# Performance work log

Hardware: AMD Instinct MI355X
Metric: run time of the kernel (lower is better)

The kernel has to match this reference:

```python
import jax, jax.numpy as jnp
import numpy as np

PI = 3.141592653589793
EPSILON = 1e-3
USE_TANH = True


def setup_inputs() -> dict:
    key = jax.random.key(0)
    k1, k2, k3, k4, k5 = jax.random.split(key, 5)
    b, t, d, p = 4, 8192, 64, 8
    return {
        "query": jax.random.normal(k1, (b, t, d), dtype=jnp.float32),
        "W_Q": jax.random.normal(k2, (p, d), dtype=jnp.float32),
        "W_K": jax.random.normal(k3, (p, d), dtype=jnp.float32),
        "W_V": jax.random.normal(k4, (p, d, d), dtype=jnp.float32),
        "W_O": jax.random.uniform(k5, (p,), dtype=jnp.float32),
    }


def reference(query, W_Q, W_K, W_V, W_O):
    # key = value = query (decoder-only self-attention usage)
    q = jnp.einsum("bti,pi->btp", query, W_Q)
    k = jnp.einsum("bti,pi->btp", query, W_K)
    V = jnp.einsum("bti,pio->btpo", query, W_V)  # (b,t,p,o)
    if USE_TANH:
        q = jnp.tanh(q) * (PI / 4)
        k = jnp.tanh(k) * (PI / 4)
    cos_k = jnp.cos(k)[..., None]  # (b,t,p,1)
    sin_k = jnp.sin(k)[..., None]
    # causal prefix sums over time (axis=-3)
    cos_KV = jnp.cumsum(cos_k * V, axis=-3)
    sin_KV = jnp.cumsum(sin_k * V, axis=-3)
    cos_Q = jnp.cos(q)[..., None]
    sin_Q = jnp.sin(q)[..., None]
    heads = cos_Q * cos_KV + sin_Q * sin_KV  # (b,t,p,o)
    cos_K = jnp.cumsum(cos_k, axis=-3)
    sin_K = jnp.cumsum(sin_k, axis=-3)
    denom = cos_Q * cos_K + sin_Q * sin_K + EPSILON
    heads = heads / denom
    return jnp.einsum("btpo,p->bto", heads, W_O)
```

## Files before the change

### kernel.cpp

```cpp
#include <hip/hip_runtime.h>
#include <hip/hip_bf16.h>
#include <math.h>

#define BB  4
#define TT  8192
#define DD  64
#define PP  8
#define CC  32
#define NCH (TT/CC)
#define AGG_STRIDE 130
#define QSTR 68

#define EPSV 1e-3f
#define KPI4 0.78539816339744830962f

typedef __attribute__((ext_vector_type(8))) short short8;
typedef __attribute__((ext_vector_type(4))) float f32x4;

__device__ __forceinline__ float bf2f(unsigned short h) {
  return __uint_as_float(((unsigned)h) << 16);
}
__device__ __forceinline__ unsigned short f2bf(float f) {
  unsigned u = __float_as_uint(f);
  u += 0x7fffu + ((u >> 16) & 1u);
  return (unsigned short)(u >> 16);
}
__device__ __forceinline__ float fast_tanh(float x) {
  float e = __expf(2.f * x);
  return 1.f - 2.f * __builtin_amdgcn_rcpf(e + 1.f);
}

__global__ __launch_bounds__(256) void k_pass1(const float* __restrict__ q,
                                               const float* __restrict__ Wk,
                                               const float* __restrict__ Wv,
                                               float* __restrict__ agg,
                                               unsigned short* __restrict__ WvTh,
                                               unsigned short* __restrict__ WvTl) {
  const int blk = blockIdx.x;
  const int c = blk & (NCH - 1);
  const int b = blk >> 8;

  __shared__ float SH[64 * QSTR];
  __shared__ float Wks[PP * DD];
  __shared__ float2 kts[PP * 32];

  const int tid = threadIdx.x;
  const float* qb = q + ((size_t)b * TT + (size_t)c * CC) * DD;
  for (int g = tid; g < CC * DD; g += 256) SH[(g >> 6) * QSTR + (g & 63)] = qb[g];
  for (int g = tid; g < PP * DD; g += 256) Wks[g] = Wk[g];
  __syncthreads();

  {
    const int t = tid & 31, p = tid >> 5;
    float dk = 0.f;
    const float4* qr = (const float4*)&SH[t * QSTR];
    const float4* wr = (const float4*)&Wks[p * DD];
#pragma unroll
    for (int j = 0; j < 16; ++j) {
      float4 qv = qr[j], wv = wr[j];
      dk = fmaf(qv.x, wv.x, dk); dk = fmaf(qv.y, wv.y, dk);
      dk = fmaf(qv.z, wv.z, dk); dk = fmaf(qv.w, wv.w, dk);
    }
    float ang = fast_tanh(dk) * KPI4;
    float ck = __cosf(ang), sk = __sinf(ang);
    kts[p * 32 + t] = make_float2(ck, sk);
    float rc = ck, rs = sk;
#pragma unroll
    for (int d = 16; d >= 1; d >>= 1) {
      rc += __shfl_xor(rc, d, 32);
      rs += __shfl_xor(rs, d, 32);
    }
    if (t == 0)
      *(float2*)(agg + (size_t)((b * PP + p) * NCH + c) * AGG_STRIDE + 128) =
          make_float2(rc, rs);
  }
  __syncthreads();

  {
    const int i = tid & 63, pq = tid >> 6;
    const int p0 = pq, p1 = pq + 4;
    float c0 = 0, s0 = 0, c1 = 0, s1 = 0;
#pragma unroll
    for (int t = 0; t < CC; ++t) {
      float qv = SH[t * QSTR + i];
      float2 k0v = kts[p0 * 32 + t];
      float2 k1v = kts[p1 * 32 + t];
      c0 = fmaf(k0v.x, qv, c0);
      s0 = fmaf(k0v.y, qv, s0);
      c1 = fmaf(k1v.x, qv, c1);
      s1 = fmaf(k1v.y, qv, s1);
    }
    float* a0 = agg + (size_t)((b * PP + p0) * NCH + c) * AGG_STRIDE;
    float* a1 = agg + (size_t)((b * PP + p1) * NCH + c) * AGG_STRIDE;
    a0[i] = c0; a0[64 + i] = s0;
    a1[i] = c1; a1[64 + i] = s1;
  }

  if (blk < 64) {
    __syncthreads();
    const int k0 = blk * 8;
#pragma unroll
    for (int r = 0; r < 2; ++r) {
      int idx = tid + r * 256;
      int kk = idx >> 6, o = idx & 63;
      SH[o * QSTR + kk] = Wv[(size_t)(k0 + kk) * DD + o];
    }
    __syncthreads();
#pragma unroll
    for (int r = 0; r < 2; ++r) {
      int idx = tid + r * 256;
      int o = idx >> 3, kk = idx & 7;
      float wv = SH[o * QSTR + kk];
      unsigned short hi = f2bf(wv);
      WvTh[(size_t)o * 512 + k0 + kk] = hi;
      WvTl[(size_t)o * 512 + k0 + kk] = f2bf(wv - bf2f(hi));
    }
  }
}

__global__ __launch_bounds__(576) void k_pass2(float* __restrict__ agg) {
  const int bp = blockIdx.x;
  const int tid = threadIdx.x;
  __shared__ float totals[4][132];

  const bool act = tid < 520;
  int seg = 0, m = 0;
  float* base = agg;
  float vals[64];
  if (act) {
    seg = tid / 130;
    m = tid - seg * 130;
    base = agg + (size_t)bp * NCH * AGG_STRIDE + m;
    float run = 0.f;
#pragma unroll
    for (int u = 0; u < 64; ++u) vals[u] = base[(size_t)(seg * 64 + u) * AGG_STRIDE];
#pragma unroll
    for (int u = 0; u < 64; ++u) run += vals[u];
    totals[seg][m] = run;
  }
  __syncthreads();
  if (act) {
    float r2 = 0.f;
    for (int s = 0; s < seg; ++s) r2 += totals[s][m];
#pragma unroll
    for (int u = 0; u < 64; ++u) {
      float v = vals[u];
      base[(size_t)(seg * 64 + u) * AGG_STRIDE] = r2;
      r2 += v;
    }
  }
}

__global__ __launch_bounds__(256, 3) void k_pass3(
    const float* __restrict__ q, const float* __restrict__ Wq,
    const float* __restrict__ Wk, const float* __restrict__ Wo,
    const float* __restrict__ pref,
    const unsigned short* __restrict__ WvTh,
    const unsigned short* __restrict__ WvTl,
    float* __restrict__ out) {
  const int blk = blockIdx.x;
  const int c = blk & (NCH - 1);
  const int b = blk >> 8;

  __shared__ float Qs[CC * QSTR];
  __shared__ float Wqs[PP * DD], Wks[PP * DD];
  __shared__ float2 kts[PP * 32];
  __shared__ float2 abt[PP * 32];
  __shared__ __align__(16) short Zh[CC * 256];
  __shared__ __align__(16) short Zl[CC * 256];

  const int tid = threadIdx.x;
  const int w = tid >> 6, l = tid & 63;
  const int lm = l & 15, lg = l >> 4;
  const int oc = w << 4;

  short8 bhf[8], blf[8];
  {
    const unsigned short* ph_ = WvTh + (size_t)(oc + lm) * 512 + lg * 8;
    const unsigned short* pl_ = WvTl + (size_t)(oc + lm) * 512 + lg * 8;
#pragma unroll
    for (int kk = 0; kk < 8; ++kk) {
      bhf[kk] = *(const short8*)(ph_ + kk * 32);
      blf[kk] = *(const short8*)(pl_ + kk * 32);
    }
  }

  const float* qb = q + ((size_t)b * TT + (size_t)c * CC) * DD;
  for (int g = tid; g < CC * DD; g += 256) Qs[(g >> 6) * QSTR + (g & 63)] = qb[g];
  for (int g = tid; g < PP * DD; g += 256) { Wqs[g] = Wq[g]; Wks[g] = Wk[g]; }
  __syncthreads();

  {
    const int t = tid & 31, p = tid >> 5;
    float dq = 0.f, dk = 0.f;
    const float4* qr  = (const float4*)&Qs[t * QSTR];
    const float4* wqr = (const float4*)&Wqs[p * DD];
    const float4* wkr = (const float4*)&Wks[p * DD];
#pragma unroll
    for (int j = 0; j < 16; ++j) {
      float4 qv = qr[j], w0 = wqr[j], w1 = wkr[j];
      dq = fmaf(qv.x, w0.x, dq); dq = fmaf(qv.y, w0.y, dq);
      dq = fmaf(qv.z, w0.z, dq); dq = fmaf(qv.w, w0.w, dq);
      dk = fmaf(qv.x, w1.x, dk); dk = fmaf(qv.y, w1.y, dk);
      dk = fmaf(qv.z, w1.z, dk); dk = fmaf(qv.w, w1.w, dk);
    }
    float ang = fast_tanh(dq) * KPI4;
    float cq = __cosf(ang), sq = __sinf(ang);
    ang = fast_tanh(dk) * KPI4;
    float ck = __cosf(ang), sk = __sinf(ang);
    kts[p * 32 + t] = make_float2(ck, sk);

    float rc = ck, rs = sk;
#pragma unroll
    for (int d = 1; d < 32; d <<= 1) {
      float tc = __shfl_up(rc, (unsigned)d, 32);
      float ts = __shfl_up(rs, (unsigned)d, 32);
      if (t >= d) { rc += tc; rs += ts; }
    }
    const float* pr = pref + (size_t)((b * PP + p) * NCH + c) * AGG_STRIDE;
    rc += pr[128]; rs += pr[129];
    float den = fmaf(cq, rc, fmaf(sq, rs, EPSV));
    float ws = Wo[p] * __builtin_amdgcn_rcpf(den);
    abt[p * 32 + t] = make_float2(ws * cq, ws * sq);
  }
  __syncthreads();

  char* zbaseH = (char*)Zh;
  char* zbaseL = (char*)Zl;
  f32x4 acc0 = {0, 0, 0, 0}, acc1 = {0, 0, 0, 0};

#pragma unroll
  for (int h = 0; h < 2; ++h) {
    {
      const int p = h * 4 + w;
      const float* prC = pref + (size_t)((b * PP + p) * NCH + c) * AGG_STRIDE;
      float Ac = prC[l], As = prC[64 + l];
      const int kb = (w * 64 + l) * 2;
#pragma unroll 8
      for (int t = 0; t < CC; ++t) {
        float qv = Qs[t * QSTR + l];
        float2 ks = kts[p * 32 + t];
        float2 ab = abt[p * 32 + t];
        Ac = fmaf(ks.x, qv, Ac);
        As = fmaf(ks.y, qv, As);
        float z = fmaf(ab.x, Ac, ab.y * As);
        unsigned u = __float_as_uint(z);
        unsigned r = u + 0x7fffu + ((u >> 16) & 1u);
        const int ad = (t << 9) + (kb ^ (t << 4));
        *(short*)(zbaseH + ad) = (short)(r >> 16);
        float lo = z - __uint_as_float(r & 0xffff0000u);
        *(short*)(zbaseL + ad) = (short)(__float_as_uint(lo) >> 16);
      }
    }
    __syncthreads();
#pragma unroll
    for (int kk = 0; kk < 8; ++kk) {
      const int base = kk * 64 + lg * 16;
      const int rb0 = (lm << 9) + (base ^ (lm << 4));
      const int rb1 = ((16 + lm) << 9) + (base ^ ((16 + lm) << 4));
      short8 ah0 = *(const short8*)(zbaseH + rb0);
      short8 al0 = *(const short8*)(zbaseL + rb0);
      short8 ah1 = *(const short8*)(zbaseH + rb1);
      short8 al1 = *(const short8*)(zbaseL + rb1);
      acc0 = __builtin_amdgcn_mfma_f32_16x16x32_bf16(ah0, bhf[kk], acc0, 0, 0, 0);
      acc1 = __builtin_amdgcn_mfma_f32_16x16x32_bf16(ah1, bhf[kk], acc1, 0, 0, 0);
      acc0 = __builtin_amdgcn_mfma_f32_16x16x32_bf16(al0, bhf[kk], acc0, 0, 0, 0);
      acc1 = __builtin_amdgcn_mfma_f32_16x16x32_bf16(al1, bhf[kk], acc1, 0, 0, 0);
      acc0 = __builtin_amdgcn_mfma_f32_16x16x32_bf16(ah0, blf[kk], acc0, 0, 0, 0);
      acc1 = __builtin_amdgcn_mfma_f32_16x16x32_bf16(ah1, blf[kk], acc1, 0, 0, 0);
    }
    if (h == 0) {
      const unsigned short* ph_ = WvTh + (size_t)(oc + lm) * 512 + 256 + lg * 8;
      const unsigned short* pl_ = WvTl + (size_t)(oc + lm) * 512 + 256 + lg * 8;
#pragma unroll
      for (int kk = 0; kk < 8; ++kk) {
        bhf[kk] = *(const short8*)(ph_ + kk * 32);
        blf[kk] = *(const short8*)(pl_ + kk * 32);
      }
    }
    __syncthreads();
  }

  {
    float* ob = out + ((size_t)b * TT + (size_t)c * CC + lg * 4) * DD + oc + lm;
#pragma unroll
    for (int r = 0; r < 4; ++r) {
      ob[r * DD] = acc0[r];
      ob[(16 + r) * DD] = acc1[r];
    }
  }
}

extern "C" void kernel_launch(void* const* d_in, const int* in_sizes, int n_in,
                              void* d_out, int out_size, void* d_ws, size_t ws_size,
                              hipStream_t stream) {
  const float* q  = (const float*)d_in[0];
  const float* Wq = (const float*)d_in[1];
  const float* Wk = (const float*)d_in[2];
  const float* Wv = (const float*)d_in[3];
  const float* Wo = (const float*)d_in[4];
  float* out = (float*)d_out;
  float* agg = (float*)d_ws;
  unsigned short* WvTh = (unsigned short*)(agg + (size_t)BB * PP * NCH * AGG_STRIDE);
  unsigned short* WvTl = WvTh + (size_t)512 * 64;

  k_pass1<<<BB * NCH, 256, 0, stream>>>(q, Wk, Wv, agg, WvTh, WvTl);
  k_pass2<<<BB * PP, 576, 0, stream>>>(agg);
  k_pass3<<<BB * NCH, 256, 0, stream>>>(q, Wq, Wk, Wo, agg, WvTh, WvTl, out);
}
```

Before: 44.80 us.

## Broadcast per-head cos/sin via readlane instead of LDS tables, drop barriers

Remaps head-to-wave assignment so each wave owns heads 2w and 2w+1. Their per-timestep cos/sin and alpha/beta values then sit in the same wave's registers and are broadcast with readlane, instead of going through shared-memory tables. This removes the kts/abt LDS arrays and two block-wide barriers in both kernels, plus the final barrier after the second MFMA half. The Wv transpose layout in pass1 is permuted to match the new head ordering in pass3. The cost is many scalar readlane operations inside the inner loops.

```diff
diff --git a/kernel.cpp b/kernel.cpp
--- a/kernel.cpp
+++ b/kernel.cpp
@@ -28,6 +28,9 @@
 __device__ __forceinline__ float fast_tanh(float x) {
   float e = __expf(2.f * x);
   return 1.f - 2.f * __builtin_amdgcn_rcpf(e + 1.f);
+}
+__device__ __forceinline__ float rlane(float v, int lane) {
+  return __uint_as_float(__builtin_amdgcn_readlane(__float_as_uint(v), lane));
 }
 
 __global__ __launch_bounds__(256) void k_pass1(const float* __restrict__ q,
@@ -42,14 +45,15 @@
 
   __shared__ float SH[64 * QSTR];
   __shared__ float Wks[PP * DD];
-  __shared__ float2 kts[PP * 32];
 
   const int tid = threadIdx.x;
+  const int w = tid >> 6, l = tid & 63;
   const float* qb = q + ((size_t)b * TT + (size_t)c * CC) * DD;
   for (int g = tid; g < CC * DD; g += 256) SH[(g >> 6) * QSTR + (g & 63)] = qb[g];
   for (int g = tid; g < PP * DD; g += 256) Wks[g] = Wk[g];
   __syncthreads();
 
+  float ckR, skR;
   {
     const int t = tid & 31, p = tid >> 5;
     float dk = 0.f;
@@ -62,9 +66,8 @@
       dk = fmaf(qv.z, wv.z, dk); dk = fmaf(qv.w, wv.w, dk);
     }
     float ang = fast_tanh(dk) * KPI4;
-    float ck = __cosf(ang), sk = __sinf(ang);
-    kts[p * 32 + t] = make_float2(ck, sk);
-    float rc = ck, rs = sk;
+    ckR = __cosf(ang); skR = __sinf(ang);
+    float rc = ckR, rs = skR;
 #pragma unroll
     for (int d = 16; d >= 1; d >>= 1) {
       rc += __shfl_xor(rc, d, 32);
@@ -74,21 +77,18 @@
       *(float2*)(agg + (size_t)((b * PP + p) * NCH + c) * AGG_STRIDE + 128) =
           make_float2(rc, rs);
   }
-  __syncthreads();
-
-  {
-    const int i = tid & 63, pq = tid >> 6;
-    const int p0 = pq, p1 = pq + 4;
+
+  {
+    const int i = l;
+    const int p0 = 2 * w, p1 = 2 * w + 1;
     float c0 = 0, s0 = 0, c1 = 0, s1 = 0;
 #pragma unroll
     for (int t = 0; t < CC; ++t) {
       float qv = SH[t * QSTR + i];
-      float2 k0v = kts[p0 * 32 + t];
-      float2 k1v = kts[p1 * 32 + t];
-      c0 = fmaf(k0v.x, qv, c0);
-      s0 = fmaf(k0v.y, qv, s0);
-      c1 = fmaf(k1v.x, qv, c1);
-      s1 = fmaf(k1v.y, qv, s1);
+      c0 = fmaf(rlane(ckR, t), qv, c0);
+      s0 = fmaf(rlane(skR, t), qv, s0);
+      c1 = fmaf(rlane(ckR, t + 32), qv, c1);
+      s1 = fmaf(rlane(skR, t + 32), qv, s1);
     }
     float* a0 = agg + (size_t)((b * PP + p0) * NCH + c) * AGG_STRIDE;
     float* a1 = agg + (size_t)((b * PP + p1) * NCH + c) * AGG_STRIDE;
@@ -110,10 +110,13 @@
     for (int r = 0; r < 2; ++r) {
       int idx = tid + r * 256;
       int o = idx >> 3, kk = idx & 7;
+      int k = k0 + kk;
+      int p = k >> 6, i = k & 63;
+      int col = ((p & 1) << 8) + ((p >> 1) << 6) + i;
       float wv = SH[o * QSTR + kk];
       unsigned short hi = f2bf(wv);
-      WvTh[(size_t)o * 512 + k0 + kk] = hi;
-      WvTl[(size_t)o * 512 + k0 + kk] = f2bf(wv - bf2f(hi));
+      WvTh[(size_t)o * 512 + col] = hi;
+      WvTl[(size_t)o * 512 + col] = f2bf(wv - bf2f(hi));
     }
   }
 }
@@ -164,8 +167,6 @@
 
   __shared__ float Qs[CC * QSTR];
   __shared__ float Wqs[PP * DD], Wks[PP * DD];
-  __shared__ float2 kts[PP * 32];
-  __shared__ float2 abt[PP * 32];
   __shared__ __align__(16) short Zh[CC * 256];
   __shared__ __align__(16) short Zl[CC * 256];
 
@@ -190,6 +191,7 @@
   for (int g = tid; g < PP * DD; g += 256) { Wqs[g] = Wq[g]; Wks[g] = Wk[g]; }
   __syncthreads();
 
+  float ckR, skR, alR, beR;
   {
     const int t = tid & 31, p = tid >> 5;
     float dq = 0.f, dk = 0.f;
@@ -207,10 +209,9 @@
     float ang = fast_tanh(dq) * KPI4;
     float cq = __cosf(ang), sq = __sinf(ang);
     ang = fast_tanh(dk) * KPI4;
-    float ck = __cosf(ang), sk = __sinf(ang);
-    kts[p * 32 + t] = make_float2(ck, sk);
-
-    float rc = ck, rs = sk;
+    ckR = __cosf(ang); skR = __sinf(ang);
+
+    float rc = ckR, rs = skR;
 #pragma unroll
     for (int d = 1; d < 32; d <<= 1) {
       float tc = __shfl_up(rc, (unsigned)d, 32);
@@ -221,9 +222,8 @@
     rc += pr[128]; rs += pr[129];
     float den = fmaf(cq, rc, fmaf(sq, rs, EPSV));
     float ws = Wo[p] * __builtin_amdgcn_rcpf(den);
-    abt[p * 32 + t] = make_float2(ws * cq, ws * sq);
-  }
-  __syncthreads();
+    alR = ws * cq; beR = ws * sq;
+  }
 
   char* zbaseH = (char*)Zh;
   char* zbaseL = (char*)Zl;
@@ -232,18 +232,19 @@
 #pragma unroll
   for (int h = 0; h < 2; ++h) {
     {
-      const int p = h * 4 + w;
+      const int p = 2 * w + h;
       const float* prC = pref + (size_t)((b * PP + p) * NCH + c) * AGG_STRIDE;
       float Ac = prC[l], As = prC[64 + l];
       const int kb = (w * 64 + l) * 2;
+      const int ls = h << 5;
 #pragma unroll 8
       for (int t = 0; t < CC; ++t) {
         float qv = Qs[t * QSTR + l];
-        float2 ks = kts[p * 32 + t];
-        float2 ab = abt[p * 32 + t];
-        Ac = fmaf(ks.x, qv, Ac);
-        As = fmaf(ks.y, qv, As);
-        float z = fmaf(ab.x, Ac, ab.y * As);
+        float ck = rlane(ckR, t + ls), sk = rlane(skR, t + ls);
+        float al = rlane(alR, t + ls), be = rlane(beR, t + ls);
+        Ac = fmaf(ck, qv, Ac);
+        As = fmaf(sk, qv, As);
+        float z = fmaf(al, Ac, be * As);
         unsigned u = __float_as_uint(z);
         unsigned r = u + 0x7fffu + ((u >> 16) & 1u);
         const int ad = (t << 9) + (kb ^ (t << 4));
@@ -277,8 +278,8 @@
         bhf[kk] = *(const short8*)(ph_ + kk * 32);
         blf[kk] = *(const short8*)(pl_ + kk * 32);
       }
-    }
-    __syncthreads();
+      __syncthreads();
+    }
   }
 
   {
```

Result: no change. 45.67 us (+1.9%).
